# Optimization experiments

Measured on AMD Instinct MI355X. Metric: run time of the kernel, lower is better.

The kernel has to match this reference:

```python
import jax, jax.numpy as jnp
import numpy as np

NUM_HEADS = 16
EPS = 1e-6


def setup_inputs() -> dict:
    key = jax.random.key(0)
    k1, k2, k3 = jax.random.split(key, 3)
    B, S, D = 4, 4096, 1024
    x = jax.random.normal(k1, (B, S, D), dtype=jnp.float32)
    # weights scaled like nn.Linear init (~1/sqrt(fan_in))
    Wqkv = jax.random.normal(k2, (D, 3 * D), dtype=jnp.float32) / np.sqrt(D)
    Wo = jax.random.normal(k3, (D, D), dtype=jnp.float32) / np.sqrt(D)
    return {"x": x, "Wqkv": Wqkv, "Wo": Wo}


def reference(x, Wqkv, Wo):
    B, S, D = x.shape
    H = NUM_HEADS
    hd = D // H
    qkv = x @ Wqkv                                   # [B,S,3D]
    qkv = qkv.reshape(B, S, 3, H, hd).transpose(2, 0, 3, 1, 4)
    Q, K, V = qkv[0], qkv[1], qkv[2]                 # [B,H,S,hd]
    # feature map: elu(x) + 1 (positive)
    Q = jax.nn.elu(Q) + 1.0
    K = jax.nn.elu(K) + 1.0
    # O(N d^2): KV state then Q contraction
    KV = jnp.einsum('bhnd,bhnv->bhdv', K, V)         # [B,H,hd,hd]
    out = jnp.einsum('bhnd,bhdv->bhnv', Q, KV)       # [B,H,S,hd]
    K_sum = K.sum(axis=2)                            # [B,H,hd]
    normalizer = jnp.einsum('bhnd,bhd->bhn', Q, K_sum)[..., None]  # [B,H,S,1]
    out = out / (normalizer + EPS)
    out = out.transpose(0, 2, 1, 3).reshape(B, S, D)
    return out @ Wo
```

## Files before the change

### kernel.cpp

```cpp
#include <hip/hip_runtime.h>

using u16 = unsigned short;
typedef __attribute__((ext_vector_type(8))) short short8;
typedef __attribute__((ext_vector_type(4))) float f32x4;

__device__ __forceinline__ u16 f2bf(float f) {
  unsigned int u = __float_as_uint(f);
  u = (u + 0x7FFFu + ((u >> 16) & 1u)) >> 16;
  return (u16)u;
}
__device__ __forceinline__ float bf2f(u16 v) {
  return __uint_as_float(((unsigned int)v) << 16);
}

__device__ __forceinline__ void gload16(const void* g, void* l) {
  __builtin_amdgcn_global_load_lds((const __attribute__((address_space(1))) void*)g,
                                   (__attribute__((address_space(3))) void*)l, 16, 0, 0);
}

#define B_ 4
#define S_ 4096
#define D_ 1024
#define H_ 16
#define HD_ 64
#define M_ (B_*S_)
#define N1_ (3*D_)

#define OFF_XB    0ull
#define OFF_WQKVT (OFF_XB    + (size_t)M_*D_*2)
#define OFF_WOT   (OFF_WQKVT + (size_t)N1_*D_*2)
#define OFF_QBUF  (OFF_WOT   + (size_t)D_*D_*2)
#define OFF_KT    (OFF_QBUF  + (size_t)M_*D_*2)
#define OFF_VT    (OFF_KT    + (size_t)M_*D_*2)
#define OFF_KV    (OFF_VT    + (size_t)M_*D_*2)
#define OFF_KSUM  (OFF_KV    + (size_t)4*64*4096*4)
#define WS_NEEDED (OFF_KSUM  + (size_t)4*64*64*4)
#define OFF_WT    OFF_KT
#define OFF_KSG   (OFF_KT + ((size_t)9<<20))
#define OFF_KVPP  OFF_VT
#define OFF_KSPP  (OFF_VT + ((size_t)16<<20))

__global__ __launch_bounds__(256) void prep_kernel(const float* __restrict__ x, u16* __restrict__ xb,
                                                   const float* __restrict__ Wqkv, u16* __restrict__ wqkvt,
                                                   const float* __restrict__ Wo, u16* __restrict__ wot)
{
  __shared__ float tile[32][33];
  int bid = blockIdx.x, tid = threadIdx.x;
  if (bid < 16384) {
    int i = bid * 256 + tid;
    float4 v = ((const float4*)x)[i];
    uint2 o;
    o.x = (unsigned)f2bf(v.x) | ((unsigned)f2bf(v.y) << 16);
    o.y = (unsigned)f2bf(v.z) | ((unsigned)f2bf(v.w) << 16);
    ((uint2*)xb)[i] = o;
    return;
  }
  const float* in; u16* out; int R, C, cb, rb;
  if (bid < 19456) {
    int t = bid - 16384;  in = Wqkv; out = wqkvt; R = D_; C = N1_;
    cb = t % 96; rb = t / 96;
  } else {
    int t = bid - 19456;  in = Wo; out = wot; R = D_; C = D_;
    cb = t % 32; rb = t / 32;
  }
  int tx = tid & 31, ty = tid >> 5;
  int c0 = cb * 32, r0 = rb * 32;
#pragma unroll
  for (int i = 0; i < 4; i++)
    tile[ty + i*8][tx] = in[(size_t)(r0 + ty + i*8) * C + c0 + tx];
  __syncthreads();
#pragma unroll
  for (int i = 0; i < 4; i++)
    out[(size_t)(c0 + ty + i*8) * R + r0 + tx] = f2bf(tile[tx][ty + i*8]);
}

template<int MODE>
__global__ __launch_bounds__(512, 2) void gemm256(
    const u16* __restrict__ A, const u16* __restrict__ Bt,
    float* __restrict__ Cf, u16* __restrict__ qout,
    float* __restrict__ P1, float* __restrict__ P2,
    const float* __restrict__ Ks,
    int M, int N, int K)
{
  __shared__ __align__(16) char smem[131072];
  int tid = threadIdx.x;
  int w = tid >> 6, lane = tid & 63;
  int quad = lane >> 4, l16 = lane & 15;
  int wm = w >> 2, wn = w & 3;

  int nwg = gridDim.x * gridDim.y;
  int flat = blockIdx.y * gridDim.x + blockIdx.x;
  int wg = (flat & 7) * (nwg >> 3) + (flat >> 3);
  int bx = wg % gridDim.x, by = wg / gridDim.x;
  int bm = by * 256, bn = bx * 256;

  int prl = lane >> 3;
  int c4  = (lane & 7) ^ prl;
  int r0  = ((w << 3) + prl) * 2 + (c4 >> 2);
  int koff = (c4 & 3) * 8;
  const u16* gA0 = A + (size_t)(bm + r0) * K + koff;
  const u16* gB0;
  size_t rowskipA = (size_t)128 * K;
  size_t rowskipB;
  if constexpr (MODE == 3) {
    gB0 = Bt + (size_t)(1024 + bx * 128 + r0) * K + koff;
    rowskipB = (size_t)1024 * K;
  } else if constexpr (MODE == 2) {
    gB0 = Bt + ((size_t)(bm >> 12) << 20) + (size_t)(bn + r0) * K + koff;
    rowskipB = (size_t)128 * K;
  } else {
    gB0 = Bt + (size_t)(bn + r0) * K + koff;
    rowskipB = (size_t)128 * K;
  }
  char* smemc = smem;
  int ldsAw = w * 1024;
  int ldsBw = 65536 + w * 1024;

  int ph = (((l16 & 1) << 2) | quad) ^ ((l16 >> 1) & 7);
  int baseA = wm * 8192 + (l16 >> 1) * 128 + ph * 16;
  int baseB = 65536 + wn * 4096 + (l16 >> 1) * 128 + ph * 16;

  f32x4 acc[8][4];
#pragma unroll
  for (int i = 0; i < 8; i++)
#pragma unroll
    for (int j = 0; j < 4; j++) acc[i][j] = (f32x4)0.0f;

  int nt = K >> 5;

#define STG(tt, slot) {                                                   \
    const u16* a0_ = gA0 + (tt) * 32;                                     \
    const u16* b0_ = gB0 + (tt) * 32;                                     \
    gload16(a0_,            smemc + (slot)*16384 + ldsAw);                \
    gload16(a0_ + rowskipA, smemc + (slot)*16384 + 8192 + ldsAw);         \
    gload16(b0_,            smemc + (slot)*16384 + ldsBw);                \
    gload16(b0_ + rowskipB, smemc + (slot)*16384 + 8192 + ldsBw);         \
  }

#define COMPUTE(slot) {                                                              \
    const char* sb = smemc + (slot) * 16384;                                         \
    short8 bfr[4], af[8];                                                            \
    _Pragma("unroll")                                                                \
    for (int nj = 0; nj < 4; nj++) bfr[nj] = *(const short8*)(sb + baseB + nj*1024); \
    _Pragma("unroll")                                                                \
    for (int mi = 0; mi < 8; mi++) af[mi] = *(const short8*)(sb + baseA + mi*1024);  \
    __builtin_amdgcn_s_setprio(1);                                                   \
    _Pragma("unroll")                                                                \
    for (int mi = 0; mi < 8; mi++)                                                   \
      _Pragma("unroll")                                                              \
      for (int nj = 0; nj < 4; nj++)                                                 \
        acc[mi][nj] = __builtin_amdgcn_mfma_f32_16x16x32_bf16(af[mi], bfr[nj],       \
                                                              acc[mi][nj], 0, 0, 0); \
    __builtin_amdgcn_s_setprio(0);                                                   \
  }

#define WAITBAR(n) {                                                      \
    asm volatile("s_waitcnt vmcnt(" #n ")" ::: "memory");                 \
    __builtin_amdgcn_s_barrier();                                         \
    asm volatile("" ::: "memory");                                        \
  }

  STG(0, 0); STG(1, 1); STG(2, 2);
  WAITBAR(8)

  for (int tb = 0; tb < nt - 4; tb += 4) {
#pragma unroll
    for (int i = 0; i < 4; ++i) {
      int t = tb + i;
      STG(t + 3, ((i + 3) & 3));
      COMPUTE(i)
      WAITBAR(8)
    }
  }

  STG(nt - 1, 3);
  COMPUTE(0)
  WAITBAR(8)
  COMPUTE(1)
  WAITBAR(4)
  COMPUTE(2)
  WAITBAR(0)
  COMPUTE(3)

#undef STG
#undef COMPUTE
#undef WAITBAR

  if constexpr (MODE == 2) {
    int colbase = bn + wn * 64;
#pragma unroll
    for (int mi = 0; mi < 8; mi++) {
      int row0 = bm + wm * 128 + mi * 16 + quad * 4;
#pragma unroll
      for (int nj = 0; nj < 4; nj++) {
        int col = colbase + nj * 16 + l16;
#pragma unroll
        for (int r = 0; r < 4; r++)
          Cf[(size_t)(row0 + r) * N + col] = acc[mi][nj][r];
      }
    }
  } else if constexpr (MODE == 4) {
    int colbase = bn + wn * 64;
    int b = bm >> 12;
    int h = colbase >> 6;
    float ksv[4];
#pragma unroll
    for (int nj = 0; nj < 4; nj++)
      ksv[nj] = Ks[(b * 16 + h) * 64 + nj * 16 + l16];
#pragma unroll
    for (int mi = 0; mi < 8; mi++) {
      float vv[4][4], nrm[4];
#pragma unroll
      for (int r = 0; r < 4; r++) nrm[r] = 0.0f;
#pragma unroll
      for (int nj = 0; nj < 4; nj++)
#pragma unroll
        for (int r = 0; r < 4; r++) {
          float v = acc[mi][nj][r];
          v = (v > 0.0f) ? (v + 1.0f) : __expf(v);
          vv[nj][r] = v;
          nrm[r] += v * ksv[nj];
        }
#pragma unroll
      for (int r = 0; r < 4; r++) {
        nrm[r] += __shfl_xor(nrm[r], 1);
        nrm[r] += __shfl_xor(nrm[r], 2);
        nrm[r] += __shfl_xor(nrm[r], 4);
        nrm[r] += __shfl_xor(nrm[r], 8);
        nrm[r] = 1.0f / (nrm[r] + 1e-6f);
      }
      int row0 = bm + wm * 128 + mi * 16 + quad * 4;
#pragma unroll
      for (int nj = 0; nj < 4; nj++) {
        int col = colbase + nj * 16 + l16;
#pragma unroll
        for (int r = 0; r < 4; r++)
          qout[(size_t)(row0 + r) * D_ + col] = f2bf(vv[nj][r] * nrm[r]);
      }
    }
  } else {
    __syncthreads();
    {
      char* basekv = smemc + ((wn < 2) ? 0 : 65536);
      bool doElu = (wn < 2);
#pragma unroll
      for (int mi = 0; mi < 8; mi++) {
        int sb = wm * 128 + mi * 16 + quad * 4;
        int slot = sb >> 5;
        int kc = (sb >> 3) & 3;
        int so = (sb & 7) * 2;
#pragma unroll
        for (int nj = 0; nj < 4; nj++) {
          int dv = (wn & 1) * 64 + nj * 16 + l16;
          int pc = (((dv & 1) << 2) | kc) ^ ((dv >> 1) & 7);
          float v0 = acc[mi][nj][0], v1 = acc[mi][nj][1], v2 = acc[mi][nj][2], v3 = acc[mi][nj][3];
          if (doElu) {
            v0 = (v0 > 0.0f) ? (v0 + 1.0f) : __expf(v0);
            v1 = (v1 > 0.0f) ? (v1 + 1.0f) : __expf(v1);
            v2 = (v2 > 0.0f) ? (v2 + 1.0f) : __expf(v2);
            v3 = (v3 > 0.0f) ? (v3 + 1.0f) : __expf(v3);
          }
          uint2 o;
          o.x = (unsigned)f2bf(v0) | ((unsigned)f2bf(v1) << 16);
          o.y = (unsigned)f2bf(v2) | ((unsigned)f2bf(v3) << 16);
          *(uint2*)(basekv + slot*8192 + (dv >> 1)*128 + pc*16 + so) = o;
        }
      }
    }
    __syncthreads();
    int hh = w >> 2, dh = w & 1, vh = (w >> 1) & 1;
    short8 ones;
#pragma unroll
    for (int e = 0; e < 8; ++e) ones[e] = (short)0x3F80;
    f32x4 a2[2][2], s2[2];
#pragma unroll
    for (int i = 0; i < 2; i++) {
      s2[i] = (f32x4)0.0f;
#pragma unroll
      for (int j = 0; j < 2; j++) a2[i][j] = (f32x4)0.0f;
    }
#pragma unroll
    for (int t = 0; t < 8; t++) {
      short8 ak[2], bv[2];
#pragma unroll
      for (int i = 0; i < 2; i++) {
        int d = hh * 64 + dh * 32 + i * 16 + l16;
        ak[i] = *(const short8*)(smemc + t*8192 + (d >> 1)*128 +
                                 (((((d & 1) << 2) | quad)) ^ ((d >> 1) & 7))*16);
        int v = hh * 64 + vh * 32 + i * 16 + l16;
        bv[i] = *(const short8*)(smemc + 65536 + t*8192 + (v >> 1)*128 +
                                 (((((v & 1) << 2) | quad)) ^ ((v >> 1) & 7))*16);
      }
#pragma unroll
      for (int i = 0; i < 2; i++) {
#pragma unroll
        for (int j = 0; j < 2; j++)
          a2[i][j] = __builtin_amdgcn_mfma_f32_16x16x32_bf16(ak[i], bv[j], a2[i][j], 0, 0, 0);
        if (vh == 0)
          s2[i] = __builtin_amdgcn_mfma_f32_16x16x32_bf16(ak[i], ones, s2[i], 0, 0, 0);
      }
    }
    int p = bx;
    int mb = bm >> 8;
    float* kdst = P1 + (size_t)(mb * 16 + p * 2 + hh) * 4096;
#pragma unroll
    for (int i = 0; i < 2; i++)
#pragma unroll
      for (int j = 0; j < 2; j++)
#pragma unroll
        for (int r = 0; r < 4; r++)
          kdst[(dh*32 + i*16 + quad*4 + r) * 64 + vh*32 + j*16 + l16] = a2[i][j][r];
    if (vh == 0 && l16 == 0) {
      float* sdst = P2 + (size_t)(mb * 16 + p * 2 + hh) * 64;
#pragma unroll
      for (int i = 0; i < 2; i++)
#pragma unroll
        for (int r = 0; r < 4; r++)
          sdst[dh*32 + i*16 + quad*4 + r] = s2[i][r];
    }
  }
}

__global__ __launch_bounds__(512) void kvw_kernel(const float* __restrict__ kvpp,
                                                  const float* __restrict__ kspp,
                                                  const u16* __restrict__ wot,
                                                  u16* __restrict__ wt,
                                                  float* __restrict__ ksg)
{
  __shared__ u16 kvlds[4096];
  int tid = threadIdx.x, bh = blockIdx.x;
  int b = bh >> 4, h = bh & 15;
  for (int i = tid; i < 4096; i += 512) {
    float s = 0.0f;
#pragma unroll
    for (int m = 0; m < 16; ++m)
      s += kvpp[(size_t)(((b * 16 + m) * 16) + h) * 4096 + i];
    kvlds[i] = f2bf(s);
  }
  if (tid < 64) {
    float s = 0.0f;
#pragma unroll
    for (int m = 0; m < 16; ++m)
      s += kspp[(size_t)(((b * 16 + m) * 16) + h) * 64 + tid];
    ksg[bh * 64 + tid] = s;
  }
  __syncthreads();
  int w = tid >> 6, lane = tid & 63, quad = lane >> 4, l16 = lane & 15;

  short8 bfr[2][4];
#pragma unroll
  for (int ks = 0; ks < 2; ++ks)
#pragma unroll
    for (int nj = 0; nj < 4; ++nj)
      bfr[ks][nj] = *(const short8*)(&kvlds[(nj*16 + l16) * 64 + ks*32 + quad*8]);

  u16* dst = wt + ((size_t)b << 20);
#pragma unroll
  for (int cc = 0; cc < 4; ++cc) {
    int c0 = w * 128 + cc * 32;
    f32x4 acc[2][4];
#pragma unroll
    for (int i = 0; i < 2; i++)
#pragma unroll
      for (int j = 0; j < 4; j++) acc[i][j] = (f32x4)0.0f;
#pragma unroll
    for (int ks = 0; ks < 2; ++ks) {
#pragma unroll
      for (int mi = 0; mi < 2; ++mi) {
        short8 af = *(const short8*)(wot + (size_t)(c0 + mi*16 + l16) * 1024 + h*64 + ks*32 + quad*8);
#pragma unroll
        for (int nj = 0; nj < 4; ++nj)
          acc[mi][nj] = __builtin_amdgcn_mfma_f32_16x16x32_bf16(af, bfr[ks][nj], acc[mi][nj], 0, 0, 0);
      }
    }
#pragma unroll
    for (int mi = 0; mi < 2; ++mi) {
      int c = c0 + mi*16 + quad*4;
#pragma unroll
      for (int nj = 0; nj < 4; ++nj) {
        int hd = h*64 + nj*16 + l16;
#pragma unroll
        for (int r = 0; r < 4; ++r)
          dst[(size_t)(c + r) * 1024 + hd] = f2bf(acc[mi][nj][r]);
      }
    }
  }
}

extern "C" void kernel_launch(void* const* d_in, const int* in_sizes, int n_in,
                              void* d_out, int out_size, void* d_ws, size_t ws_size,
                              hipStream_t stream) {
  const float* x    = (const float*)d_in[0];
  const float* Wqkv = (const float*)d_in[1];
  const float* Wo   = (const float*)d_in[2];
  float* out = (float*)d_out;
  char* ws = (char*)d_ws;
  if (ws_size < WS_NEEDED) return;

  u16*   xb    = (u16*)  (ws + OFF_XB);
  u16*   wqkvt = (u16*)  (ws + OFF_WQKVT);
  u16*   wot   = (u16*)  (ws + OFF_WOT);
  u16*   qbuf  = (u16*)  (ws + OFF_QBUF);
  u16*   wt    = (u16*)  (ws + OFF_WT);
  float* ksg   = (float*)(ws + OFF_KSG);
  float* kvpp  = (float*)(ws + OFF_KVPP);
  float* kspp  = (float*)(ws + OFF_KSPP);

  prep_kernel<<<20480, 256, 0, stream>>>(x, xb, Wqkv, wqkvt, Wo, wot);
  gemm256<3><<<dim3(8, M_/256), 512, 0, stream>>>(xb, wqkvt, nullptr, nullptr, kvpp, kspp,
                                                  nullptr, M_, N1_, D_);
  kvw_kernel<<<64, 512, 0, stream>>>(kvpp, kspp, wot, wt, ksg);
  gemm256<4><<<dim3(4, M_/256), 512, 0, stream>>>(xb, wqkvt, nullptr, qbuf, nullptr, nullptr,
                                                  ksg, M_, N1_, D_);
  gemm256<2><<<dim3(4, M_/256), 512, 0, stream>>>(qbuf, wt, out, nullptr, nullptr, nullptr,
                                                  nullptr, M_, D_, D_);
}
```

Before: 288.7 us.

## Fuse KV reduction and Wo projection into KV GEMM via last-block atomic counter

Removes the separate kvw_kernel launch. Each KV-GEMM block now bumps an atomic counter per (batch, head-pair). The last block to finish reduces the 16 partial KV and Ksum slices, then computes the KV·Wo product for its two heads. The counter is zeroed by an extra block in prep_kernel. This saves a launch and its tail bubble, but the reduction and MFMA work becomes serialized on a few last-arriving blocks, and it depends on threadfence ordering being correct.

```diff
diff --git a/kernel.cpp b/kernel.cpp
--- a/kernel.cpp
+++ b/kernel.cpp
@@ -39,13 +39,19 @@
 #define OFF_KSG   (OFF_KT + ((size_t)9<<20))
 #define OFF_KVPP  OFF_VT
 #define OFF_KSPP  (OFF_VT + ((size_t)16<<20))
+#define OFF_CNT   (OFF_VT + ((size_t)17<<20))
 
 __global__ __launch_bounds__(256) void prep_kernel(const float* __restrict__ x, u16* __restrict__ xb,
                                                    const float* __restrict__ Wqkv, u16* __restrict__ wqkvt,
-                                                   const float* __restrict__ Wo, u16* __restrict__ wot)
+                                                   const float* __restrict__ Wo, u16* __restrict__ wot,
+                                                   int* __restrict__ cnt)
 {
   __shared__ float tile[32][33];
   int bid = blockIdx.x, tid = threadIdx.x;
+  if (bid >= 20480) {
+    if (tid < 32) cnt[tid] = 0;
+    return;
+  }
   if (bid < 16384) {
     int i = bid * 256 + tid;
     float4 v = ((const float4*)x)[i];
@@ -80,9 +86,12 @@
     float* __restrict__ Cf, u16* __restrict__ qout,
     float* __restrict__ P1, float* __restrict__ P2,
     const float* __restrict__ Ks,
+    const u16* __restrict__ wotp, u16* __restrict__ wtp,
+    float* __restrict__ ksgp, int* __restrict__ cnt,
     int M, int N, int K)
 {
   __shared__ __align__(16) char smem[131072];
+  __shared__ int lastFlag;
   int tid = threadIdx.x;
   int w = tid >> 6, lane = tid & 63;
   int quad = lane >> 4, l16 = lane & 15;
@@ -302,6 +311,7 @@
     }
     int p = bx;
     int mb = bm >> 8;
+    int b = bm >> 12;
     float* kdst = P1 + (size_t)(mb * 16 + p * 2 + hh) * 4096;
 #pragma unroll
     for (int i = 0; i < 2; i++)
@@ -318,70 +328,71 @@
         for (int r = 0; r < 4; r++)
           sdst[dh*32 + i*16 + quad*4 + r] = s2[i][r];
     }
-  }
-}
-
-__global__ __launch_bounds__(512) void kvw_kernel(const float* __restrict__ kvpp,
-                                                  const float* __restrict__ kspp,
-                                                  const u16* __restrict__ wot,
-                                                  u16* __restrict__ wt,
-                                                  float* __restrict__ ksg)
-{
-  __shared__ u16 kvlds[4096];
-  int tid = threadIdx.x, bh = blockIdx.x;
-  int b = bh >> 4, h = bh & 15;
-  for (int i = tid; i < 4096; i += 512) {
-    float s = 0.0f;
-#pragma unroll
-    for (int m = 0; m < 16; ++m)
-      s += kvpp[(size_t)(((b * 16 + m) * 16) + h) * 4096 + i];
-    kvlds[i] = f2bf(s);
-  }
-  if (tid < 64) {
-    float s = 0.0f;
-#pragma unroll
-    for (int m = 0; m < 16; ++m)
-      s += kspp[(size_t)(((b * 16 + m) * 16) + h) * 64 + tid];
-    ksg[bh * 64 + tid] = s;
-  }
-  __syncthreads();
-  int w = tid >> 6, lane = tid & 63, quad = lane >> 4, l16 = lane & 15;
-
-  short8 bfr[2][4];
-#pragma unroll
-  for (int ks = 0; ks < 2; ++ks)
-#pragma unroll
-    for (int nj = 0; nj < 4; ++nj)
-      bfr[ks][nj] = *(const short8*)(&kvlds[(nj*16 + l16) * 64 + ks*32 + quad*8]);
-
-  u16* dst = wt + ((size_t)b << 20);
-#pragma unroll
-  for (int cc = 0; cc < 4; ++cc) {
-    int c0 = w * 128 + cc * 32;
-    f32x4 acc[2][4];
-#pragma unroll
-    for (int i = 0; i < 2; i++)
-#pragma unroll
-      for (int j = 0; j < 4; j++) acc[i][j] = (f32x4)0.0f;
-#pragma unroll
-    for (int ks = 0; ks < 2; ++ks) {
-#pragma unroll
-      for (int mi = 0; mi < 2; ++mi) {
-        short8 af = *(const short8*)(wot + (size_t)(c0 + mi*16 + l16) * 1024 + h*64 + ks*32 + quad*8);
+    __threadfence();
+    if (tid == 0) lastFlag = (atomicAdd(&cnt[b * 8 + p], 1) == 15);
+    __syncthreads();
+    if (!lastFlag) return;
+    __threadfence();
+    u16* kv2 = (u16*)smemc;
+    for (int i = tid; i < 8192; i += 512) {
+      int hh2 = i >> 12, idx = i & 4095;
+      float s = 0.0f;
+#pragma unroll
+      for (int m = 0; m < 16; ++m)
+        s += P1[(size_t)(((b * 16 + m) * 16) + p * 2 + hh2) * 4096 + idx];
+      kv2[i] = f2bf(s);
+    }
+    if (tid < 128) {
+      int hh2 = tid >> 6, d = tid & 63;
+      float s = 0.0f;
+#pragma unroll
+      for (int m = 0; m < 16; ++m)
+        s += P2[(size_t)(((b * 16 + m) * 16) + p * 2 + hh2) * 64 + d];
+      ksgp[(b * 16 + p * 2 + hh2) * 64 + d] = s;
+    }
+    __syncthreads();
+    u16* dst = wtp + ((size_t)b << 20);
+#pragma unroll
+    for (int hh2 = 0; hh2 < 2; ++hh2) {
+      const u16* kvl = kv2 + hh2 * 4096;
+      int hg = p * 2 + hh2;
+      short8 bfr2[2][4];
+#pragma unroll
+      for (int ks = 0; ks < 2; ++ks)
 #pragma unroll
         for (int nj = 0; nj < 4; ++nj)
-          acc[mi][nj] = __builtin_amdgcn_mfma_f32_16x16x32_bf16(af, bfr[ks][nj], acc[mi][nj], 0, 0, 0);
-      }
-    }
-#pragma unroll
-    for (int mi = 0; mi < 2; ++mi) {
-      int c = c0 + mi*16 + quad*4;
-#pragma unroll
-      for (int nj = 0; nj < 4; ++nj) {
-        int hd = h*64 + nj*16 + l16;
-#pragma unroll
-        for (int r = 0; r < 4; ++r)
-          dst[(size_t)(c + r) * 1024 + hd] = f2bf(acc[mi][nj][r]);
+          bfr2[ks][nj] = *(const short8*)(&kvl[(nj*16 + l16) * 64 + ks*32 + quad*8]);
+#pragma unroll
+      for (int cc = 0; cc < 4; ++cc) {
+        int c0 = w * 128 + cc * 32;
+        f32x4 acc2[2][4];
+#pragma unroll
+        for (int i = 0; i < 2; i++)
+#pragma unroll
+          for (int j = 0; j < 4; j++) acc2[i][j] = (f32x4)0.0f;
+#pragma unroll
+        for (int ks = 0; ks < 2; ++ks) {
+#pragma unroll
+          for (int mi = 0; mi < 2; ++mi) {
+            short8 af2 = *(const short8*)(wotp + (size_t)(c0 + mi*16 + l16) * 1024
+                                          + hg*64 + ks*32 + quad*8);
+#pragma unroll
+            for (int nj = 0; nj < 4; ++nj)
+              acc2[mi][nj] = __builtin_amdgcn_mfma_f32_16x16x32_bf16(af2, bfr2[ks][nj],
+                                                                     acc2[mi][nj], 0, 0, 0);
+          }
+        }
+#pragma unroll
+        for (int mi = 0; mi < 2; ++mi) {
+          int c = c0 + mi*16 + quad*4;
+#pragma unroll
+          for (int nj = 0; nj < 4; ++nj) {
+            int hd = hg*64 + nj*16 + l16;
+#pragma unroll
+            for (int r = 0; r < 4; ++r)
+              dst[(size_t)(c + r) * 1024 + hd] = f2bf(acc2[mi][nj][r]);
+          }
+        }
       }
     }
   }
@@ -405,13 +416,15 @@
   float* ksg   = (float*)(ws + OFF_KSG);
   float* kvpp  = (float*)(ws + OFF_KVPP);
   float* kspp  = (float*)(ws + OFF_KSPP);
-
-  prep_kernel<<<20480, 256, 0, stream>>>(x, xb, Wqkv, wqkvt, Wo, wot);
+  int*   cnt   = (int*)  (ws + OFF_CNT);
+
+  prep_kernel<<<20481, 256, 0, stream>>>(x, xb, Wqkv, wqkvt, Wo, wot, cnt);
   gemm256<3><<<dim3(8, M_/256), 512, 0, stream>>>(xb, wqkvt, nullptr, nullptr, kvpp, kspp,
-                                                  nullptr, M_, N1_, D_);
-  kvw_kernel<<<64, 512, 0, stream>>>(kvpp, kspp, wot, wt, ksg);
+                                                  nullptr, wot, wt, ksg, cnt, M_, N1_, D_);
   gemm256<4><<<dim3(4, M_/256), 512, 0, stream>>>(xb, wqkvt, nullptr, qbuf, nullptr, nullptr,
-                                                  ksg, M_, N1_, D_);
+                                                  ksg, nullptr, nullptr, nullptr, nullptr,
+                                                  M_, N1_, D_);
   gemm256<2><<<dim3(4, M_/256), 512, 0, stream>>>(qbuf, wt, out, nullptr, nullptr, nullptr,
-                                                  nullptr, M_, D_, D_);
-}
+                                                  nullptr, nullptr, nullptr, nullptr, nullptr,
+                                                  M_, D_, D_);
+}
```

After: 415.3 us. 1.44x slower.
